# Performance work log

Measured on AMD Instinct MI355X. Metric: run time of the kernel, lower is better.

## Reference

```python
import jax, jax.numpy as jnp
import numpy as np

EMBED_DIM = 1024
NUM_HEADS = 16
HEAD_DIM = EMBED_DIM // NUM_HEADS
SCALE = HEAD_DIM ** -0.5


def setup_inputs() -> dict:
    key = jax.random.key(0)
    k_x, k_qkv, k_w, k_b = jax.random.split(key, 4)
    B, N = 2, 2048
    x = jax.random.normal(k_x, (B, N, EMBED_DIM), dtype=jnp.float32)
    # nn.Linear weights stored as (out, in); init with small normal
    w_qkv = jax.random.normal(k_qkv, (3 * EMBED_DIM, EMBED_DIM), dtype=jnp.float32) * (EMBED_DIM ** -0.5)
    w_out = jax.random.normal(k_w, (EMBED_DIM, EMBED_DIM), dtype=jnp.float32) * (EMBED_DIM ** -0.5)
    b_out = jax.random.normal(k_b, (EMBED_DIM,), dtype=jnp.float32) * 0.02
    return {"x": x, "w_qkv": w_qkv, "w_out": w_out, "b_out": b_out}


def reference(x, w_qkv, w_out, b_out):
    B, N, _ = x.shape
    # qkv: (B, N, 3*E) -> (B, N, 3, H, Dh)
    qkv = jnp.einsum('bne,fe->bnf', x, w_qkv).reshape(B, N, 3, NUM_HEADS, HEAD_DIM)
    q, k, v = qkv[:, :, 0], qkv[:, :, 1], qkv[:, :, 2]
    scores = jnp.einsum('bnhd,bmhd->bhnm', q, k) * SCALE
    attn = jax.nn.softmax(scores, axis=-1)  # dropout is identity in eval mode
    out = jnp.einsum('bhnm,bmhd->bnhd', attn, v).reshape(B, N, EMBED_DIM)
    return jnp.einsum('bne,fe->bnf', out, w_out) + b_out
```

## Files before the change

kernel.cpp:

```cpp
#include <hip/hip_runtime.h>
#include <stdint.h>
#include <stddef.h>

#define SEQ   2048
#define BATCH 2
#define NTOK  (SEQ*BATCH)
#define EMB   1024
#define QKVN  3072
#define NH    16
#define HD    64

typedef __bf16 bf16x8 __attribute__((ext_vector_type(8)));
typedef float  f32x4  __attribute__((ext_vector_type(4)));

__device__ __forceinline__ unsigned short f2b(float f) {
  union { float f; uint32_t u; } v; v.f = f;
  uint32_t r = v.u + 0x7fffu + ((v.u >> 16) & 1u);
  return (unsigned short)(r >> 16);
}

#define GLOAD_LDS16(gp, lp)                                                    \
  __builtin_amdgcn_global_load_lds(                                            \
      (__attribute__((address_space(1))) void*)(gp),                           \
      (__attribute__((address_space(3))) void*)(lp), 16, 0, 0)

__global__ void cvt_bf16_kernel(const float* __restrict__ in,
                                unsigned short* __restrict__ out, int n4) {
  int i = blockIdx.x * blockDim.x + threadIdx.x;
  if (i < n4) {
    float4 v = ((const float4*)in)[i];
    ushort4 o;
    o.x = f2b(v.x); o.y = f2b(v.y); o.z = f2b(v.z); o.w = f2b(v.w);
    ((ushort4*)out)[i] = o;
  }
}

__global__ __launch_bounds__(256) void gemm_bt(
    const unsigned short* __restrict__ A,
    const unsigned short* __restrict__ B,
    unsigned short* __restrict__ Cb,
    float* __restrict__ Cf,
    const float* __restrict__ bias,
    unsigned short* __restrict__ vt,
    int M, int N, int K, int mode)
{
  __shared__ unsigned short As[128*32];
  __shared__ unsigned short Bs[128*32];

  const int tid  = threadIdx.x;
  const int wave = tid >> 6, lane = tid & 63;
  const int l16  = lane & 15, quad = lane >> 4;
  const int tm = blockIdx.x * 128, tn = blockIdx.y * 128;
  const int wm = (wave & 1) * 64,  wn = (wave >> 1) * 64;

  f32x4 acc[4][4] = {};

  for (int k0 = 0; k0 < K; k0 += 32) {
    __syncthreads();
#pragma unroll
    for (int j = 0; j < 2; ++j) {
      const int e   = (wave*2 + j)*512 + lane*8;
      const int row = e >> 5, kk = e & 31;
      GLOAD_LDS16(A + (size_t)(tm + row)*K + (k0 + kk), As + (wave*2 + j)*512);
      GLOAD_LDS16(B + (size_t)(tn + row)*K + (k0 + kk), Bs + (wave*2 + j)*512);
    }
    __syncthreads();

    bf16x8 af[4], bf[4];
#pragma unroll
    for (int i = 0; i < 4; ++i) {
      af[i] = *(const bf16x8*)(As + (wm + i*16 + l16)*32 + quad*8);
      bf[i] = *(const bf16x8*)(Bs + (wn + i*16 + l16)*32 + quad*8);
    }
#pragma unroll
    for (int mi = 0; mi < 4; ++mi)
#pragma unroll
      for (int ni = 0; ni < 4; ++ni)
        acc[mi][ni] = __builtin_amdgcn_mfma_f32_16x16x32_bf16(af[mi], bf[ni], acc[mi][ni], 0, 0, 0);
  }

  if (mode == 1) {
#pragma unroll
    for (int mi = 0; mi < 4; ++mi)
#pragma unroll
      for (int ni = 0; ni < 4; ++ni)
#pragma unroll
        for (int r = 0; r < 4; ++r) {
          const int row = tm + wm + mi*16 + quad*4 + r;
          const int col = tn + wn + ni*16 + l16;
          Cf[(size_t)row*N + col] = acc[mi][ni][r] + bias[col];
        }
  } else {
    if (tn < 2048) {
#pragma unroll
      for (int mi = 0; mi < 4; ++mi)
#pragma unroll
        for (int ni = 0; ni < 4; ++ni)
#pragma unroll
          for (int r = 0; r < 4; ++r) {
            const int row = tm + wm + mi*16 + quad*4 + r;
            const int col = tn + wn + ni*16 + l16;
            Cb[(size_t)row*2048 + col] = f2b(acc[mi][ni][r]);
          }
    } else {
#pragma unroll
      for (int mi = 0; mi < 4; ++mi)
#pragma unroll
        for (int ni = 0; ni < 4; ++ni) {
          const int f    = tn + wn + ni*16 + l16 - 2048;
          const int row0 = tm + wm + mi*16 + quad*4;
          const int bb   = row0 >> 11;
          const int n0   = row0 & 2047;
          ushort4 pv;
          pv.x = f2b(acc[mi][ni][0]); pv.y = f2b(acc[mi][ni][1]);
          pv.z = f2b(acc[mi][ni][2]); pv.w = f2b(acc[mi][ni][3]);
          *(ushort4*)(vt + ((size_t)(bb*1024 + f))*2048 + n0) = pv;
        }
    }
  }
}

__global__ __launch_bounds__(256) void attn_kernel(
    const unsigned short* __restrict__ qk,
    const unsigned short* __restrict__ vT,
    unsigned short* __restrict__ aout)
{
  __shared__ unsigned short Ks[64*64];
  __shared__ unsigned short Vt[64*64];
  __shared__ unsigned short Pl[4*16*64];

  const int tid  = threadIdx.x;
  const int wave = tid >> 6, lane = tid & 63;
  const int l16  = lane & 15, quad = lane >> 4;

  const int flat = blockIdx.x;
  const int xcd  = flat & 7;
  const int idx  = flat >> 3;
  const int bh   = xcd*4 + (idx >> 5);
  const int qt   = idx & 31;
  const int b  = bh >> 4, h = bh & 15;
  const size_t tok0 = (size_t)b * SEQ;
  const int qrow0 = qt*64 + wave*16;
  const int swz = (l16 & 7) << 3;

  bf16x8 qf[2];
  {
    const unsigned short* qp = qk + (tok0 + qrow0 + l16)*2048 + h*64;
#pragma unroll
    for (int ks = 0; ks < 2; ++ks) {
      bf16x8 t = *(const bf16x8*)(qp + ks*32 + quad*8);
#pragma unroll
      for (int j = 0; j < 8; ++j) t[j] = (__bf16)((float)t[j] * 0.125f);
      qf[ks] = t;
    }
  }

  f32x4 oacc[4] = {};
  float l_run = 0.f;
  unsigned short* Pw = Pl + wave*(16*64);
  const float LOG2E = 1.44269504f;
  const float OFF2  = 17.3123405f;

  for (int kb = 0; kb < SEQ/64; ++kb) {
    const int kk0 = kb*64;
    __syncthreads();
#pragma unroll
    for (int j = 0; j < 2; ++j) {
      const int p    = j*256 + wave*64 + lane;
      const int row  = p >> 3;
      const int c    = (p & 7) ^ (row & 7);
      GLOAD_LDS16(qk + (tok0 + kk0 + row)*2048 + 1024 + h*64 + c*8,
                  Ks + (j*256 + wave*64)*8);
      GLOAD_LDS16(vT + ((size_t)(b*1024 + h*64 + row))*2048 + kk0 + c*8,
                  Vt + (j*256 + wave*64)*8);
    }
    __syncthreads();

    f32x4 s[4] = {};
    __builtin_amdgcn_s_setprio(1);
#pragma unroll
    for (int ks = 0; ks < 2; ++ks)
#pragma unroll
      for (int mf = 0; mf < 4; ++mf) {
        bf16x8 kf = *(const bf16x8*)(Ks + (mf*16 + l16)*64 + (((ks*4 + quad) ^ (l16 & 7)) << 3));
        s[mf] = __builtin_amdgcn_mfma_f32_16x16x32_bf16(kf, qf[ks], s[mf], 0, 0, 0);
      }
    __builtin_amdgcn_s_setprio(0);

    {
      float rs = l_run;
#pragma unroll
      for (int mf = 0; mf < 4; ++mf) {
        union { float f; uint32_t u; } a0, a1, a2, a3;
        a0.f = __builtin_amdgcn_exp2f(fmaf(s[mf][0], LOG2E, -OFF2));
        a1.f = __builtin_amdgcn_exp2f(fmaf(s[mf][1], LOG2E, -OFF2));
        a2.f = __builtin_amdgcn_exp2f(fmaf(s[mf][2], LOG2E, -OFF2));
        a3.f = __builtin_amdgcn_exp2f(fmaf(s[mf][3], LOG2E, -OFF2));
        rs += (a0.f + a1.f) + (a2.f + a3.f);
        uint2 pk;
        pk.x = __builtin_amdgcn_perm(a1.u, a0.u, 0x07060302u);
        pk.y = __builtin_amdgcn_perm(a3.u, a2.u, 0x07060302u);
        *(uint2*)(Pw + l16*64 + ((mf*16 + quad*4) ^ swz)) = pk;
      }
      l_run = rs;
    }

    __builtin_amdgcn_s_setprio(1);
#pragma unroll
    for (int ks = 0; ks < 2; ++ks) {
      bf16x8 pf = *(const bf16x8*)(Pw + l16*64 + ((ks*32 + quad*8) ^ swz));
#pragma unroll
      for (int mf = 0; mf < 4; ++mf) {
        bf16x8 vf = *(const bf16x8*)(Vt + (mf*16 + l16)*64 + (((ks*4 + quad) ^ (l16 & 7)) << 3));
        oacc[mf] = __builtin_amdgcn_mfma_f32_16x16x32_bf16(vf, pf, oacc[mf], 0, 0, 0);
      }
    }
    __builtin_amdgcn_s_setprio(0);
  }

  {
    float l = l_run;
    l += __shfl_xor(l, 16);
    l += __shfl_xor(l, 32);
    const float inv = 1.0f / l;
    const size_t trow = tok0 + qrow0 + l16;
#pragma unroll
    for (int mf = 0; mf < 4; ++mf) {
      ushort4 ov;
      ov.x = f2b(oacc[mf][0] * inv);
      ov.y = f2b(oacc[mf][1] * inv);
      ov.z = f2b(oacc[mf][2] * inv);
      ov.w = f2b(oacc[mf][3] * inv);
      *(ushort4*)(aout + trow*EMB + h*64 + mf*16 + quad*4) = ov;
    }
  }
}

extern "C" void kernel_launch(void* const* d_in, const int* in_sizes, int n_in,
                              void* d_out, int out_size, void* d_ws, size_t ws_size,
                              hipStream_t stream) {
  const float* x     = (const float*)d_in[0];
  const float* w_qkv = (const float*)d_in[1];
  const float* w_out = (const float*)d_in[2];
  const float* b_out = (const float*)d_in[3];

  char* ws = (char*)d_ws;
  unsigned short* xb    = (unsigned short*)(ws);
  unsigned short* wqkvb = (unsigned short*)(ws + 8388608);
  unsigned short* woutb = (unsigned short*)(ws + 14680064);
  unsigned short* qkb   = (unsigned short*)(ws + 16777216);
  unsigned short* vTb   = (unsigned short*)(ws + 33554432);
  unsigned short* aob   = (unsigned short*)(ws + 41943040);

  cvt_bf16_kernel<<<(NTOK*EMB/4 + 255)/256, 256, 0, stream>>>(x, xb, NTOK*EMB/4);
  cvt_bf16_kernel<<<(QKVN*EMB/4 + 255)/256, 256, 0, stream>>>(w_qkv, wqkvb, QKVN*EMB/4);
  cvt_bf16_kernel<<<(EMB*EMB/4 + 255)/256, 256, 0, stream>>>(w_out, woutb, EMB*EMB/4);

  gemm_bt<<<dim3(NTOK/128, QKVN/128), 256, 0, stream>>>(
      xb, wqkvb, qkb, nullptr, nullptr, vTb, NTOK, QKVN, EMB, 2);

  attn_kernel<<<dim3(1024), 256, 0, stream>>>(qkb, vTb, aob);

  gemm_bt<<<dim3(NTOK/128, EMB/128), 256, 0, stream>>>(
      aob, woutb, nullptr, (float*)d_out, b_out, nullptr, NTOK, EMB, EMB, 1);
}
```

Before: 208.7 us.

## Double-buffer K/V tiles in attention kernel to overlap loads with compute

Splits the shared-memory K and V tiles into two buffers. Each iteration issues async global-to-LDS loads for the next key block while it computes on the current one, and keeps a single barrier per iteration instead of two. The aim is to hide global-load latency behind the QK and PV MFMA work. In exchange, LDS use per block rises from about 24KB to about 40KB, which may lower the number of blocks resident per CU.

```diff
diff --git a/kernel.cpp b/kernel.cpp
--- a/kernel.cpp
+++ b/kernel.cpp
@@ -125,8 +125,8 @@
     const unsigned short* __restrict__ vT,
     unsigned short* __restrict__ aout)
 {
-  __shared__ unsigned short Ks[64*64];
-  __shared__ unsigned short Vt[64*64];
+  __shared__ unsigned short Ks[2][64*64];
+  __shared__ unsigned short Vt[2][64*64];
   __shared__ unsigned short Pl[4*16*64];
 
   const int tid  = threadIdx.x;
@@ -143,6 +143,23 @@
   const int qrow0 = qt*64 + wave*16;
   const int swz = (l16 & 7) << 3;
 
+  const int sp0  = wave*64 + lane;
+  const int sp1  = 256 + wave*64 + lane;
+  const int srow0 = sp0 >> 3, sc0 = ((sp0 & 7) ^ (srow0 & 7)) << 3;
+  const int srow1 = sp1 >> 3, sc1 = ((sp1 & 7) ^ (srow1 & 7)) << 3;
+  const unsigned short* kbase = qk + tok0*2048 + 1024 + h*64;
+  const unsigned short* vbase = vT + ((size_t)(b*1024 + h*64))*2048;
+  const int ldst0 = (wave*64)*8;
+  const int ldst1 = (256 + wave*64)*8;
+
+#define STAGE(dst, kk0s)                                                      \
+  do {                                                                        \
+    GLOAD_LDS16(kbase + (size_t)((kk0s) + srow0)*2048 + sc0, Ks[dst] + ldst0);\
+    GLOAD_LDS16(vbase + (size_t)srow0*2048 + (kk0s) + sc0,   Vt[dst] + ldst0);\
+    GLOAD_LDS16(kbase + (size_t)((kk0s) + srow1)*2048 + sc1, Ks[dst] + ldst1);\
+    GLOAD_LDS16(vbase + (size_t)srow1*2048 + (kk0s) + sc1,   Vt[dst] + ldst1);\
+  } while (0)
+
   bf16x8 qf[2];
   {
     const unsigned short* qp = qk + (tok0 + qrow0 + l16)*2048 + h*64;
@@ -161,20 +178,15 @@
   const float LOG2E = 1.44269504f;
   const float OFF2  = 17.3123405f;
 
+  STAGE(0, 0);
+  __syncthreads();
+
   for (int kb = 0; kb < SEQ/64; ++kb) {
-    const int kk0 = kb*64;
-    __syncthreads();
-#pragma unroll
-    for (int j = 0; j < 2; ++j) {
-      const int p    = j*256 + wave*64 + lane;
-      const int row  = p >> 3;
-      const int c    = (p & 7) ^ (row & 7);
-      GLOAD_LDS16(qk + (tok0 + kk0 + row)*2048 + 1024 + h*64 + c*8,
-                  Ks + (j*256 + wave*64)*8);
-      GLOAD_LDS16(vT + ((size_t)(b*1024 + h*64 + row))*2048 + kk0 + c*8,
-                  Vt + (j*256 + wave*64)*8);
-    }
-    __syncthreads();
+    const int cur = kb & 1;
+    if (kb + 1 < SEQ/64) STAGE(cur ^ 1, (kb + 1)*64);
+
+    const unsigned short* Kc = Ks[cur];
+    const unsigned short* Vc = Vt[cur];
 
     f32x4 s[4] = {};
     __builtin_amdgcn_s_setprio(1);
@@ -182,7 +194,7 @@
     for (int ks = 0; ks < 2; ++ks)
 #pragma unroll
       for (int mf = 0; mf < 4; ++mf) {
-        bf16x8 kf = *(const bf16x8*)(Ks + (mf*16 + l16)*64 + (((ks*4 + quad) ^ (l16 & 7)) << 3));
+        bf16x8 kf = *(const bf16x8*)(Kc + (mf*16 + l16)*64 + (((ks*4 + quad) ^ (l16 & 7)) << 3));
         s[mf] = __builtin_amdgcn_mfma_f32_16x16x32_bf16(kf, qf[ks], s[mf], 0, 0, 0);
       }
     __builtin_amdgcn_s_setprio(0);
@@ -211,12 +223,15 @@
       bf16x8 pf = *(const bf16x8*)(Pw + l16*64 + ((ks*32 + quad*8) ^ swz));
 #pragma unroll
       for (int mf = 0; mf < 4; ++mf) {
-        bf16x8 vf = *(const bf16x8*)(Vt + (mf*16 + l16)*64 + (((ks*4 + quad) ^ (l16 & 7)) << 3));
+        bf16x8 vf = *(const bf16x8*)(Vc + (mf*16 + l16)*64 + (((ks*4 + quad) ^ (l16 & 7)) << 3));
         oacc[mf] = __builtin_amdgcn_mfma_f32_16x16x32_bf16(vf, pf, oacc[mf], 0, 0, 0);
       }
     }
     __builtin_amdgcn_s_setprio(0);
-  }
+
+    __syncthreads();
+  }
+#undef STAGE
 
   {
     float l = l_run;
```

New measurement: 207.2 us. No clear change (-0.7%).
